# Kernel tuning notes

Hardware: AMD Instinct MI355X
Metric: run time of the kernel (lower is better)

## Reference

```python
import jax, jax.numpy as jnp
import numpy as np

EMB = 64  # emb_dim
T = 4     # message-passing steps


def setup_inputs() -> dict:
    key = jax.random.key(0)
    ks = jax.random.split(key, 9)
    B, N = 32, 1024
    graph = jax.random.uniform(ks[0], (B, N, N), jnp.float32)   # dense adjacency/weights
    Xv = jax.random.normal(ks[1], (B, N, 1), jnp.float32)       # per-vertex scalar feature
    s = lambda k, shp: (jax.random.normal(k, shp, jnp.float32) * 0.05)
    return {
        "graph": graph,
        "Xv": Xv,
        "W1": s(ks[2], (EMB, 1)),        # Linear(1, emb) no bias, torch layout [out, in]
        "W2": s(ks[3], (EMB, EMB)),
        "W3": s(ks[4], (EMB, EMB)),
        "W4": s(ks[5], (EMB, 1)),
        "W5": s(ks[6], (1, 2 * EMB)),
        "W6": s(ks[7], (EMB, EMB)),
        "W7": s(ks[8], (EMB, EMB)),
    }


def reference(graph, Xv, W1, W2, W3, W4, W5, W6, W7):
    B, N = Xv.shape[0], Xv.shape[1]
    # v1 = W1(Xv): [B,N,1] @ [1,EMB] -> [B,N,EMB]
    v1 = Xv @ W1.T
    # Original: v3 = W3(sum_j W4(graph[...,None])). W4 is linear (no bias), so
    # sum_j W4(g_ij) == W4(sum_j g_ij) -- exact by linearity, avoids [B,N,N,EMB] temp.
    deg = jnp.sum(graph, axis=2, keepdims=True)        # [B,N,1]
    v3 = (deg @ W4.T) @ W3.T                           # [B,N,EMB]
    base = v1 + v3                                     # loop-invariant part
    emb = jnp.zeros((B, N, EMB), dtype=Xv.dtype)
    for _ in range(T):
        neighbor_sum = jnp.einsum('bij,bjd->bid', graph, emb)  # bmm aggregation
        emb = jax.nn.relu(base + neighbor_sum @ W2.T)
    emb_sum = jnp.sum(emb, axis=1)                     # [B,EMB]
    # v6.repeat(1,N).view(B,N,EMB) == broadcast the per-graph vector to every vertex
    v6 = jnp.broadcast_to((emb_sum @ W6.T)[:, None, :], (B, N, EMB))
    v7 = emb @ W7.T
    ct = jax.nn.relu(jnp.concatenate([v6, v7], axis=2))  # [B,N,2*EMB]
    return (ct @ W5.T)[..., 0]                            # [B,N]
```

## Files before the change

kernel.cpp:

```cpp
#include <hip/hip_runtime.h>
#include <stdint.h>

#define NV 1024
#define EMB 64

typedef __attribute__((ext_vector_type(8))) short bf16x8;
typedef __attribute__((ext_vector_type(4))) float f32x4;

__device__ __forceinline__ unsigned short f2b(float f) {
  unsigned int u = __builtin_bit_cast(unsigned int, f);
  u += 0x7fffu + ((u >> 16) & 1u);
  return (unsigned short)(u >> 16);
}
__device__ __forceinline__ float b2f(unsigned short s) {
  unsigned int u = ((unsigned int)s) << 16;
  return __builtin_bit_cast(float, u);
}

__device__ __forceinline__ void gll16(void* lds, const void* gsrc) {
  __builtin_amdgcn_global_load_lds(
      (const __attribute__((address_space(1))) unsigned int*)gsrc,
      (__attribute__((address_space(3))) unsigned int*)lds, 16, 0, 0);
}

__device__ __forceinline__ void swz(int j, int& b, int& mb) {
  const int xcd = j & 7, s = j >> 3;
  b = xcd + 8 * (s >> 4);
  mb = s & 15;
}

__global__ __launch_bounds__(256) void k_prep(
    const float* __restrict__ graph, const float* __restrict__ Xv,
    const float* __restrict__ W1, const float* __restrict__ W3,
    const float* __restrict__ W4,
    unsigned short* __restrict__ G16, float* __restrict__ degp,
    float* __restrict__ w34g, unsigned short* __restrict__ embT)
{
  __shared__ float w34s[EMB];
  __shared__ __align__(16) unsigned short ebT[EMB][68];
  const int tid = threadIdx.x;
  int b, mb; swz(blockIdx.x, b, mb);
  if (tid < EMB) {
    float s = 0.f;
    const float* w3r = W3 + tid * EMB;
#pragma unroll
    for (int k = 0; k < EMB; ++k) s += w3r[k] * W4[k];
    w34s[tid] = s;
    if (blockIdx.x == 0) w34g[tid] = s;
  }
  __syncthreads();
  const int wv = tid >> 6, lane = tid & 63;
  const float w1v = W1[lane];
  const float w34v = w34s[lane];
  for (int i = 0; i < 16; ++i) {
    const int rloc = wv * 16 + i;
    const int row = mb * 64 + rloc;
    const float4* gr = (const float4*)(graph + ((size_t)b * NV + row) * NV);
    float part = 0.f;
    ushort4 outp[4];
#pragma unroll
    for (int c = 0; c < 4; ++c) {
      float4 v = gr[c * 64 + lane];
      part += (v.x + v.y) + (v.z + v.w);
      outp[c].x = f2b(v.x); outp[c].y = f2b(v.y);
      outp[c].z = f2b(v.z); outp[c].w = f2b(v.w);
    }
    ushort4* g16r = (ushort4*)(G16 + ((size_t)b * NV + row) * NV);
#pragma unroll
    for (int c = 0; c < 4; ++c) g16r[c * 64 + lane] = outp[c];
#pragma unroll
    for (int d = 1; d < 64; d <<= 1) part += __shfl_xor(part, d);
    const float deg = part;
    if (lane == 0) degp[b * NV + row] = deg;
    const float xv = Xv[b * NV + row];
    const float bs = xv * w1v + deg * w34v;
    ebT[lane][rloc] = f2b(fmaxf(bs, 0.f));
  }
  __syncthreads();
  const int e = tid >> 2, q = tid & 3;
  ushort4* dst = (ushort4*)(embT + ((size_t)(b * EMB + e)) * NV + mb * 64 + q * 16);
  const ushort4* srcr = (const ushort4*)(&ebT[e][q * 16]);
#pragma unroll
  for (int c = 0; c < 4; ++c) dst[c] = srcr[c];
}

template <int LAST>
__global__ __launch_bounds__(512, 4) void k_step(
    const unsigned short* __restrict__ G16,
    const unsigned short* __restrict__ embin,
    unsigned short* __restrict__ embout,
    const float* __restrict__ W2, const float* __restrict__ W1,
    const float* __restrict__ w34g, const float* __restrict__ Xv,
    const float* __restrict__ degp, float* __restrict__ esum_ws)
{
  __shared__ __align__(16) char ldsbuf[65536];
  __shared__ float esl[EMB];
  const int tid = threadIdx.x;
  const int lane = tid & 63;
  const int wv = tid >> 6;
  int b, mb; swz(blockIdx.x, b, mb);
  const int wm = wv >> 1;
  const int wn = wv & 1;
  const int l15 = lane & 15, l4 = lane >> 4;

  bf16x8 w2f[2][2];
  float w1e[2], w34e[2];
#pragma unroll
  for (int e16 = 0; e16 < 2; ++e16) {
    const int eg = wn * 32 + e16 * 16 + l15;
    w1e[e16] = W1[eg];
    w34e[e16] = w34g[eg];
#pragma unroll
    for (int kk = 0; kk < 2; ++kk) {
      const float* src = W2 + eg * 64 + kk * 32 + l4 * 8;
      bf16x8 f;
#pragma unroll
      for (int j = 0; j < 8; ++j) f[j] = (short)f2b(src[j]);
      w2f[e16][kk] = f;
    }
  }
  if (LAST && tid < EMB) esl[tid] = 0.f;

  f32x4 acc[2] = {};
  const size_t gbase = ((size_t)b * NV + mb * 64) * NV;
  const size_t ebase = (size_t)b * EMB * NV;

  const int lrow = tid >> 3;
  const int gcg = (tid & 7) ^ (lrow & 7);
  const size_t asrc = gbase + (size_t)lrow * NV + gcg * 8;
  const size_t bsrc = ebase + (size_t)lrow * NV + gcg * 8;

  auto STAGE = [&](int bufi, int kt) {
    char* Ad = ldsbuf + bufi * 16384;
    gll16(Ad + wv * 1024, G16 + asrc + kt * 64);
    gll16(Ad + 8192 + wv * 1024, embin + bsrc + kt * 64);
  };

  STAGE(0, 0); STAGE(1, 1); STAGE(2, 2);
  for (int kt = 0; kt < 16; ++kt) {
    if (kt < 13) {
      STAGE((kt + 3) & 3, kt + 3);
      asm volatile("s_waitcnt vmcnt(6)" ::: "memory");
    } else if (kt == 13) {
      asm volatile("s_waitcnt vmcnt(4)" ::: "memory");
    } else if (kt == 14) {
      asm volatile("s_waitcnt vmcnt(2)" ::: "memory");
    } else {
      asm volatile("s_waitcnt vmcnt(0)" ::: "memory");
    }
    __builtin_amdgcn_s_barrier();
    asm volatile("" ::: "memory");
    const char* At = ldsbuf + (kt & 3) * 16384;
    const char* Bt = At + 8192;
#pragma unroll
    for (int kk = 0; kk < 2; ++kk) {
      const int gq = kk * 4 + l4;
      const int row = wm * 16 + l15;
      const bf16x8 af = *(const bf16x8*)(At + row * 128 + ((gq ^ (row & 7)) << 4));
#pragma unroll
      for (int n16 = 0; n16 < 2; ++n16) {
        const int er = wn * 32 + n16 * 16 + l15;
        const bf16x8 bfr = *(const bf16x8*)(Bt + er * 128 + ((gq ^ (er & 7)) << 4));
        acc[n16] = __builtin_amdgcn_mfma_f32_16x16x32_bf16(af, bfr, acc[n16], 0, 0, 0);
      }
    }
    asm volatile("" ::: "memory");
    __builtin_amdgcn_s_barrier();
  }

  char* St = ldsbuf;
#pragma unroll
  for (int n16 = 0; n16 < 2; ++n16)
#pragma unroll
    for (int r = 0; r < 4; ++r) {
      const int m = wm * 16 + l4 * 4 + r;
      const int n = wn * 32 + n16 * 16 + l15;
      const int addr = m * 128 + (((n >> 3) ^ (m & 7)) << 4) + (n & 7) * 2;
      *(unsigned short*)(St + addr) = f2b(acc[n16][r]);
    }
  __syncthreads();

  f32x4 acc2[2] = {};
#pragma unroll
  for (int kk = 0; kk < 2; ++kk) {
    const int gq = kk * 4 + l4;
    const int row = wm * 16 + l15;
    const bf16x8 sa = *(const bf16x8*)(St + row * 128 + ((gq ^ (row & 7)) << 4));
#pragma unroll
    for (int e16 = 0; e16 < 2; ++e16)
      acc2[e16] = __builtin_amdgcn_mfma_f32_16x16x32_bf16(
          sa, w2f[e16][kk], acc2[e16], 0, 0, 0);
  }

  const int ml0 = wm * 16 + l4 * 4;
  const int m0 = mb * 64 + ml0;
  float xv4[4], dg4[4];
#pragma unroll
  for (int r = 0; r < 4; ++r) {
    xv4[r] = Xv[b * NV + m0 + r];
    dg4[r] = degp[b * NV + m0 + r];
  }
#pragma unroll
  for (int e16 = 0; e16 < 2; ++e16) {
    const int eg = wn * 32 + e16 * 16 + l15;
    ushort4 pk;
    unsigned short* pks = (unsigned short*)&pk;
    float evs = 0.f;
#pragma unroll
    for (int r = 0; r < 4; ++r) {
      const float bs = xv4[r] * w1e[e16] + dg4[r] * w34e[e16];
      const float val = fmaxf(acc2[e16][r] + bs, 0.f);
      pks[r] = f2b(val);
      evs += val;
    }
    *(ushort4*)(embout + ((size_t)(b * EMB + eg)) * NV + m0) = pk;
    if (LAST) atomicAdd(&esl[eg], evs);
  }
  if (LAST) {
    __syncthreads();
    if (tid < EMB) atomicAdd(&esum_ws[b * EMB + tid], esl[tid]);
  }
}

__global__ __launch_bounds__(256) void k_out(
    const unsigned short* __restrict__ embT, const float* __restrict__ W7,
    const float* __restrict__ W5, const float* __restrict__ W6,
    const float* __restrict__ esum_ws, float* __restrict__ out)
{
  __shared__ __align__(16) unsigned short et[EMB][256];
  __shared__ float s6l;
  const int tid = threadIdx.x;
  const int b = blockIdx.x >> 2;
  const int n0 = (blockIdx.x & 3) * 256;
#pragma unroll
  for (int i = 0; i < 8; ++i) {
    const int c = i * 256 + tid;
    const int k = c >> 5, off = (c & 31) * 8;
    *(uint4*)&et[k][off] =
        *(const uint4*)(embT + ((size_t)(b * EMB + k)) * NV + n0 + off);
  }
  if (tid < EMB) {
    const float* es = esum_ws + b * EMB;
    float v6 = 0.f;
    const float* w6r = W6 + tid * EMB;
#pragma unroll
    for (int k = 0; k < EMB; ++k) v6 += w6r[k] * es[k];
    float c = W5[tid] * fmaxf(v6, 0.f);
#pragma unroll
    for (int d = 1; d < 64; d <<= 1) c += __shfl_xor(c, d);
    if (tid == 0) s6l = c;
  }
  __syncthreads();
  float ev[64];
#pragma unroll
  for (int k = 0; k < 64; ++k) ev[k] = b2f(et[k][tid]);
  float s7 = 0.f;
  for (int e = 0; e < 64; ++e) {
    const float* w7r = W7 + e * 64;
    float a = 0.f;
#pragma unroll
    for (int k = 0; k < 64; ++k) a += ev[k] * w7r[k];
    s7 += W5[64 + e] * fmaxf(a, 0.f);
  }
  out[b * NV + n0 + tid] = s6l + s7;
}

extern "C" void kernel_launch(void* const* d_in, const int* in_sizes, int n_in,
                              void* d_out, int out_size, void* d_ws, size_t ws_size,
                              hipStream_t stream) {
  const float* graph = (const float*)d_in[0];
  const float* Xv = (const float*)d_in[1];
  const float* W1 = (const float*)d_in[2];
  const float* W2 = (const float*)d_in[3];
  const float* W3 = (const float*)d_in[4];
  const float* W4 = (const float*)d_in[5];
  const float* W5 = (const float*)d_in[6];
  const float* W6 = (const float*)d_in[7];
  const float* W7 = (const float*)d_in[8];
  float* out = (float*)d_out;
  char* ws = (char*)d_ws;

  unsigned short* G16 = (unsigned short*)ws;
  unsigned short* embA = (unsigned short*)(ws + (64u << 20));
  unsigned short* embB = (unsigned short*)(ws + (68u << 20));
  float* degp = (float*)(ws + (72u << 20));
  float* w34g = (float*)(ws + (72u << 20) + (128u << 10));
  float* esum_ws = (float*)(ws + (72u << 20) + (130u << 10));

  hipMemsetAsync(esum_ws, 0, 32 * EMB * sizeof(float), stream);
  k_prep<<<512, 256, 0, stream>>>(graph, Xv, W1, W3, W4, G16, degp, w34g, embA);
  k_step<0><<<512, 512, 0, stream>>>(G16, embA, embB, W2, W1, w34g, Xv, degp, esum_ws);
  k_step<0><<<512, 512, 0, stream>>>(G16, embB, embA, W2, W1, w34g, Xv, degp, esum_ws);
  k_step<1><<<512, 512, 0, stream>>>(G16, embA, embB, W2, W1, w34g, Xv, degp, esum_ws);
  k_out<<<128, 256, 0, stream>>>(embB, W7, W5, W6, esum_ws, out);
}
```

Measured before the change: 301.3 us.

## Shrink per-block tiles to launch more blocks across prep, step and output kernels

The prep kernel now handles 16 rows per block across 2048 blocks, and it zeroes the esum workspace itself instead of relying on a separate memset. The step kernel drops to 256 threads with 32-row M tiles and a 3-stage LDS pipeline in place of 4 stages, launching 1024 blocks. The output kernel splits each block's E dimension across two thread halves and reduces the partials through LDS. The aim is better occupancy and more parallelism on the memory-bound passes. The trade-off is that the shared emb B-tile is reloaded by twice as many blocks, and the pipeline is one stage shallower.

Result: slower. 307.7 us (+2.1%).

```diff
diff --git a/kernel.cpp b/kernel.cpp
--- a/kernel.cpp
+++ b/kernel.cpp
@@ -23,38 +23,41 @@
       (__attribute__((address_space(3))) unsigned int*)lds, 16, 0, 0);
 }
 
-__device__ __forceinline__ void swz(int j, int& b, int& mb) {
-  const int xcd = j & 7, s = j >> 3;
-  b = xcd + 8 * (s >> 4);
-  mb = s & 15;
-}
-
-__global__ __launch_bounds__(256) void k_prep(
+__global__ __launch_bounds__(256, 6) void k_prep(
     const float* __restrict__ graph, const float* __restrict__ Xv,
     const float* __restrict__ W1, const float* __restrict__ W3,
     const float* __restrict__ W4,
     unsigned short* __restrict__ G16, float* __restrict__ degp,
-    float* __restrict__ w34g, unsigned short* __restrict__ embT)
+    float* __restrict__ w34g, unsigned short* __restrict__ embT,
+    float* __restrict__ esum_ws)
 {
   __shared__ float w34s[EMB];
-  __shared__ __align__(16) unsigned short ebT[EMB][68];
+  __shared__ float partsT[64 * 16];
+  __shared__ float degw[16], xvw[16];
+  __shared__ unsigned short ebT[EMB][18];
   const int tid = threadIdx.x;
-  int b, mb; swz(blockIdx.x, b, mb);
+  const int j = blockIdx.x;
+  const int b = (j & 7) + 8 * (j >> 9);
+  const int rt = (j >> 3) & 63;
+  const int wv = tid >> 6, lane = tid & 63;
+
+  if (j == 0) {
+    ((float4*)esum_ws)[tid] = float4{0.f, 0.f, 0.f, 0.f};
+    ((float4*)esum_ws)[tid + 256] = float4{0.f, 0.f, 0.f, 0.f};
+  }
   if (tid < EMB) {
     float s = 0.f;
     const float* w3r = W3 + tid * EMB;
 #pragma unroll
     for (int k = 0; k < EMB; ++k) s += w3r[k] * W4[k];
     w34s[tid] = s;
-    if (blockIdx.x == 0) w34g[tid] = s;
-  }
-  __syncthreads();
-  const int wv = tid >> 6, lane = tid & 63;
-  const float w1v = W1[lane];
-  const float w34v = w34s[lane];
-  for (int i = 0; i < 16; ++i) {
-    const int rloc = wv * 16 + i;
-    const int row = mb * 64 + rloc;
+    if (j == 0) w34g[tid] = s;
+  }
+
+#pragma unroll 2
+  for (int r = 0; r < 4; ++r) {
+    const int slot = wv * 4 + r;
+    const int row = rt * 16 + slot;
     const float4* gr = (const float4*)(graph + ((size_t)b * NV + row) * NV);
     float part = 0.f;
     ushort4 outp[4];
@@ -68,24 +71,35 @@
     ushort4* g16r = (ushort4*)(G16 + ((size_t)b * NV + row) * NV);
 #pragma unroll
     for (int c = 0; c < 4; ++c) g16r[c * 64 + lane] = outp[c];
-#pragma unroll
-    for (int d = 1; d < 64; d <<= 1) part += __shfl_xor(part, d);
-    const float deg = part;
-    if (lane == 0) degp[b * NV + row] = deg;
-    const float xv = Xv[b * NV + row];
-    const float bs = xv * w1v + deg * w34v;
-    ebT[lane][rloc] = f2b(fmaxf(bs, 0.f));
-  }
-  __syncthreads();
-  const int e = tid >> 2, q = tid & 3;
-  ushort4* dst = (ushort4*)(embT + ((size_t)(b * EMB + e)) * NV + mb * 64 + q * 16);
-  const ushort4* srcr = (const ushort4*)(&ebT[e][q * 16]);
-#pragma unroll
-  for (int c = 0; c < 4; ++c) dst[c] = srcr[c];
+    partsT[lane * 16 + slot] = part;
+  }
+  __syncthreads();
+  if (tid < 16) {
+    float s = 0.f;
+#pragma unroll
+    for (int l = 0; l < 64; ++l) s += partsT[l * 16 + tid];
+    degw[tid] = s;
+    xvw[tid] = Xv[b * NV + rt * 16 + tid];
+    degp[b * NV + rt * 16 + tid] = s;
+  }
+  __syncthreads();
+  {
+    const int e = tid >> 2, q = tid & 3;
+    const float w1e = W1[e], w34e = w34s[e];
+#pragma unroll
+    for (int n = q * 4; n < q * 4 + 4; ++n)
+      ebT[e][n] = f2b(fmaxf(xvw[n] * w1e + degw[n] * w34e, 0.f));
+  }
+  __syncthreads();
+  {
+    const int e = tid >> 2, q = tid & 3;
+    *(ushort4*)(embT + ((size_t)(b * EMB + e)) * NV + rt * 16 + q * 4) =
+        *(const ushort4*)(&ebT[e][q * 4]);
+  }
 }
 
 template <int LAST>
-__global__ __launch_bounds__(512, 4) void k_step(
+__global__ __launch_bounds__(256, 4) void k_step(
     const unsigned short* __restrict__ G16,
     const unsigned short* __restrict__ embin,
     unsigned short* __restrict__ embout,
@@ -93,14 +107,15 @@
     const float* __restrict__ w34g, const float* __restrict__ Xv,
     const float* __restrict__ degp, float* __restrict__ esum_ws)
 {
-  __shared__ __align__(16) char ldsbuf[65536];
+  __shared__ __align__(16) char ldsbuf[36864];
   __shared__ float esl[EMB];
   const int tid = threadIdx.x;
   const int lane = tid & 63;
   const int wv = tid >> 6;
-  int b, mb; swz(blockIdx.x, b, mb);
-  const int wm = wv >> 1;
-  const int wn = wv & 1;
+  const int j = blockIdx.x;
+  const int b = (j & 7) + 8 * (j >> 8);
+  const int mt = (j >> 3) & 31;
+  const int wm = wv >> 1, wn = wv & 1;
   const int l15 = lane & 15, l4 = lane >> 4;
 
   bf16x8 w2f[2][2];
@@ -115,43 +130,47 @@
       const float* src = W2 + eg * 64 + kk * 32 + l4 * 8;
       bf16x8 f;
 #pragma unroll
-      for (int j = 0; j < 8; ++j) f[j] = (short)f2b(src[j]);
+      for (int jj = 0; jj < 8; ++jj) f[jj] = (short)f2b(src[jj]);
       w2f[e16][kk] = f;
     }
   }
   if (LAST && tid < EMB) esl[tid] = 0.f;
 
   f32x4 acc[2] = {};
-  const size_t gbase = ((size_t)b * NV + mb * 64) * NV;
+  const size_t gbase = ((size_t)b * NV + mt * 32) * NV;
   const size_t ebase = (size_t)b * EMB * NV;
 
-  const int lrow = tid >> 3;
-  const int gcg = (tid & 7) ^ (lrow & 7);
-  const size_t asrc = gbase + (size_t)lrow * NV + gcg * 8;
-  const size_t bsrc = ebase + (size_t)lrow * NV + gcg * 8;
+  const int arow = tid >> 3;
+  const int agcg = (tid & 7) ^ (arow & 7);
+  const size_t asrc = gbase + (size_t)arow * NV + agcg * 8;
 
   auto STAGE = [&](int bufi, int kt) {
-    char* Ad = ldsbuf + bufi * 16384;
-    gll16(Ad + wv * 1024, G16 + asrc + kt * 64);
-    gll16(Ad + 8192 + wv * 1024, embin + bsrc + kt * 64);
+    char* Ad = ldsbuf + bufi * 12288;
+    char* Bd = Ad + 4096;
+    gll16(Ad + tid * 16, G16 + asrc + kt * 64);
+#pragma unroll
+    for (int i = 0; i < 2; ++i) {
+      const int cc = i * 256 + tid;
+      const int er = cc >> 3, lcg = cc & 7;
+      const int gcg = lcg ^ (er & 7);
+      gll16(Bd + cc * 16, embin + ebase + (size_t)er * NV + kt * 64 + gcg * 8);
+    }
   };
 
-  STAGE(0, 0); STAGE(1, 1); STAGE(2, 2);
+  STAGE(0, 0); STAGE(1, 1);
   for (int kt = 0; kt < 16; ++kt) {
-    if (kt < 13) {
-      STAGE((kt + 3) & 3, kt + 3);
+    if (kt < 14) {
+      STAGE((kt + 2) % 3, kt + 2);
       asm volatile("s_waitcnt vmcnt(6)" ::: "memory");
-    } else if (kt == 13) {
-      asm volatile("s_waitcnt vmcnt(4)" ::: "memory");
     } else if (kt == 14) {
-      asm volatile("s_waitcnt vmcnt(2)" ::: "memory");
+      asm volatile("s_waitcnt vmcnt(3)" ::: "memory");
     } else {
       asm volatile("s_waitcnt vmcnt(0)" ::: "memory");
     }
     __builtin_amdgcn_s_barrier();
     asm volatile("" ::: "memory");
-    const char* At = ldsbuf + (kt & 3) * 16384;
-    const char* Bt = At + 8192;
+    const char* At = ldsbuf + (kt % 3) * 12288;
+    const char* Bt = At + 4096;
 #pragma unroll
     for (int kk = 0; kk < 2; ++kk) {
       const int gq = kk * 4 + l4;
@@ -193,7 +212,7 @@
   }
 
   const int ml0 = wm * 16 + l4 * 4;
-  const int m0 = mb * 64 + ml0;
+  const int m0 = mt * 32 + ml0;
   float xv4[4], dg4[4];
 #pragma unroll
   for (int r = 0; r < 4; ++r) {
@@ -227,15 +246,16 @@
     const float* __restrict__ W5, const float* __restrict__ W6,
     const float* __restrict__ esum_ws, float* __restrict__ out)
 {
-  __shared__ __align__(16) unsigned short et[EMB][256];
+  __shared__ __align__(16) unsigned short et[EMB][128];
+  __shared__ float redl[256];
   __shared__ float s6l;
   const int tid = threadIdx.x;
-  const int b = blockIdx.x >> 2;
-  const int n0 = (blockIdx.x & 3) * 256;
-#pragma unroll
-  for (int i = 0; i < 8; ++i) {
+  const int b = blockIdx.x >> 3;
+  const int n0 = (blockIdx.x & 7) * 128;
+#pragma unroll
+  for (int i = 0; i < 4; ++i) {
     const int c = i * 256 + tid;
-    const int k = c >> 5, off = (c & 31) * 8;
+    const int k = c >> 4, off = (c & 15) * 8;
     *(uint4*)&et[k][off] =
         *(const uint4*)(embT + ((size_t)(b * EMB + k)) * NV + n0 + off);
   }
@@ -251,18 +271,22 @@
     if (tid == 0) s6l = c;
   }
   __syncthreads();
+  const int v = tid & 127, eh = tid >> 7;
   float ev[64];
 #pragma unroll
-  for (int k = 0; k < 64; ++k) ev[k] = b2f(et[k][tid]);
-  float s7 = 0.f;
-  for (int e = 0; e < 64; ++e) {
+  for (int k = 0; k < 64; ++k) ev[k] = b2f(et[k][v]);
+  float sp = 0.f;
+  for (int e = eh * 32; e < eh * 32 + 32; ++e) {
     const float* w7r = W7 + e * 64;
     float a = 0.f;
 #pragma unroll
     for (int k = 0; k < 64; ++k) a += ev[k] * w7r[k];
-    s7 += W5[64 + e] * fmaxf(a, 0.f);
-  }
-  out[b * NV + n0 + tid] = s6l + s7;
+    sp += W5[64 + e] * fmaxf(a, 0.f);
+  }
+  redl[tid] = sp;
+  __syncthreads();
+  if (tid < 128)
+    out[b * NV + n0 + tid] = s6l + redl[tid] + redl[tid + 128];
 }
 
 extern "C" void kernel_launch(void* const* d_in, const int* in_sizes, int n_in,
@@ -287,10 +311,10 @@
   float* w34g = (float*)(ws + (72u << 20) + (128u << 10));
   float* esum_ws = (float*)(ws + (72u << 20) + (130u << 10));
 
-  hipMemsetAsync(esum_ws, 0, 32 * EMB * sizeof(float), stream);
-  k_prep<<<512, 256, 0, stream>>>(graph, Xv, W1, W3, W4, G16, degp, w34g, embA);
-  k_step<0><<<512, 512, 0, stream>>>(G16, embA, embB, W2, W1, w34g, Xv, degp, esum_ws);
-  k_step<0><<<512, 512, 0, stream>>>(G16, embB, embA, W2, W1, w34g, Xv, degp, esum_ws);
-  k_step<1><<<512, 512, 0, stream>>>(G16, embA, embB, W2, W1, w34g, Xv, degp, esum_ws);
-  k_out<<<128, 256, 0, stream>>>(embB, W7, W5, W6, esum_ws, out);
-}
+  k_prep<<<2048, 256, 0, stream>>>(graph, Xv, W1, W3, W4, G16, degp, w34g,
+                                   embA, esum_ws);
+  k_step<0><<<1024, 256, 0, stream>>>(G16, embA, embB, W2, W1, w34g, Xv, degp, esum_ws);
+  k_step<0><<<1024, 256, 0, stream>>>(G16, embB, embA, W2, W1, w34g, Xv, degp, esum_ws);
+  k_step<1><<<1024, 256, 0, stream>>>(G16, embA, embB, W2, W1, w34g, Xv, degp, esum_ws);
+  k_out<<<256, 256, 0, stream>>>(embB, W7, W5, W6, esum_ws, out);
+}
```
